# Performance work log

Measured on AMD Instinct MI355X. Metric: run time of the kernel, lower is better.

## Reference

```python
import jax, jax.numpy as jnp
import numpy as np

B, T, D = 16, 2048, 1024
NUM_LAYERS = 4
BN_EPS = 1e-5


def setup_inputs() -> dict:
    key = jax.random.key(0)
    ks = jax.random.split(key, 8)
    s = 1.0 / np.sqrt(D)
    x = jax.random.normal(ks[0], (B, T, D), dtype=jnp.float32)
    Wi = jax.random.normal(ks[1], (D, D), dtype=jnp.float32) * s   # SimpleCell input dense kernel
    bi = jnp.zeros((D,), dtype=jnp.float32)                         # SimpleCell input dense bias
    Wh = jax.random.normal(ks[2], (D, D), dtype=jnp.float32) * s   # recurrent dense kernel (no bias)
    mlp_W = jax.random.normal(ks[3], (NUM_LAYERS, D, D), dtype=jnp.float32) * s
    mlp_b = jnp.zeros((NUM_LAYERS, D), dtype=jnp.float32)
    bn_scale = jnp.ones((NUM_LAYERS, D), dtype=jnp.float32)
    bn_bias = jnp.zeros((NUM_LAYERS, D), dtype=jnp.float32)
    return {"x": x, "Wi": Wi, "bi": bi, "Wh": Wh,
            "mlp_W": mlp_W, "mlp_b": mlp_b,
            "bn_scale": bn_scale, "bn_bias": bn_bias}


def reference(x, Wi, bi, Wh, mlp_W, mlp_b, bn_scale, bn_bias):
    # --- linear recurrence (SimpleCell with identity activation) ---
    # h_t = (x_t @ Wi + bi) + h_{t-1} @ Wh,  h_0 = 0
    xp = jnp.einsum('btd,dh->bth', x, Wi) + bi          # pre-project inputs [B,T,H]

    def step(h, xt):
        h = xt + h @ Wh
        return h, h

    h0 = jnp.zeros((x.shape[0], Wh.shape[0]), dtype=x.dtype)
    _, ys = jax.lax.scan(step, h0, jnp.swapaxes(xp, 0, 1))  # scan over time
    y = jnp.swapaxes(ys, 0, 1)                               # [B,T,H]

    # --- residual MLP stack: gelu(BatchNorm(Linear(y))) + y ---
    n_layers = mlp_W.shape[0]
    for l in range(n_layers):
        z = jnp.einsum('bth,hk->btk', y, mlp_W[l]) + mlp_b[l]
        mean = jnp.mean(z, axis=(0, 1))
        var = jnp.var(z, axis=(0, 1))
        zn = (z - mean) * jax.lax.rsqrt(var + BN_EPS) * bn_scale[l] + bn_bias[l]
        y = jax.nn.gelu(zn) + y
    return y
```

## Files before the change

### kernel.cpp

```cpp
#include <hip/hip_runtime.h>
#include <math.h>

#define Bb   16
#define Tt   2048
#define Dd   1024
#define NL   4
#define MTOT (Bb * Tt)

typedef float f32x4 __attribute__((ext_vector_type(4)));
typedef short bf16x8 __attribute__((ext_vector_type(8)));

__device__ __forceinline__ unsigned short f2bf_rne(float x) {
    unsigned u = __float_as_uint(x);
    u += 0x7fffu + ((u >> 16) & 1u);
    return (unsigned short)(u >> 16);
}
__device__ __forceinline__ float bf2f(unsigned short h) {
    return __uint_as_float(((unsigned)h) << 16);
}
__device__ __forceinline__ float gelu_tanh(float x) {
    float x3 = x * x * x;
    float u  = 0.7978845608028654f * (x + 0.044715f * x3);
    return 0.5f * x * (1.0f + tanhf(u));
}
__device__ __forceinline__ void dma16(const void* g, void* l) {
    __builtin_amdgcn_global_load_lds(
        (const __attribute__((address_space(1))) unsigned int*)g,
        (__attribute__((address_space(3))) unsigned int*)l, 16, 0, 0);
}

__global__ __launch_bounds__(256)
void split_bt(const float* __restrict__ B, short* __restrict__ ht,
              short* __restrict__ lt)
{
    __shared__ float tile[32][33];
    const int t  = threadIdx.x;
    const int r  = t >> 3;
    const int c  = (t & 7) * 4;
    const int kb = blockIdx.y * 32;
    const int nb = blockIdx.x * 32;
    float4 v = *reinterpret_cast<const float4*>(
        &B[(size_t)(kb + r) * Dd + nb + c]);
    tile[r][c + 0] = v.x; tile[r][c + 1] = v.y;
    tile[r][c + 2] = v.z; tile[r][c + 3] = v.w;
    __syncthreads();
    unsigned h[4], lo[4];
#pragma unroll
    for (int q = 0; q < 4; ++q) {
        float f = tile[c + q][r];
        unsigned short hh = f2bf_rne(f);
        float rem = f - bf2f(hh);
        h[q]  = hh;
        lo[q] = f2bf_rne(rem);
    }
    uint2 hw, lw;
    hw.x = h[0]  | (h[1]  << 16); hw.y = h[2]  | (h[3]  << 16);
    lw.x = lo[0] | (lo[1] << 16); lw.y = lo[2] | (lo[3] << 16);
    const int n = nb + r;
    const int s = (c >> 3) ^ ((n >> 1) & 3);
    size_t off = ((size_t)(blockIdx.y * 1024 + n) * 4 + s) * 8 + (c & 4);
    *reinterpret_cast<uint2*>(&ht[off]) = hw;
    *reinterpret_cast<uint2*>(&lt[off]) = lw;
}

template<int MODE, int BN, int NT>
__global__ __launch_bounds__(256, 2)
void mfma_gemm(const float* __restrict__ A,
               const short* __restrict__ Bth, const short* __restrict__ Btl,
               const float* __restrict__ bias,
               const float* __restrict__ Sin,
               float* __restrict__ Cout,
               float* __restrict__ psum, float* __restrict__ psq,
               int m, int tstart)
{
    constexpr int NJ  = NT / 32;
    constexpr int BH  = 10240;
    constexpr int BPL = NT * 32;
    __shared__ __align__(16) short lds[BH + 2 * BPL];
    float* bnF = (float*)lds;

    const int tid  = threadIdx.x;
    const int lane = tid & 63;
    const int w    = tid >> 6;
    const int n0   = blockIdx.x * NT;
    const int m0g  = (MODE == 2) ? (blockIdx.y * Tt + tstart)
                                 : (blockIdx.y * 128);
    const int wm0  = (w >> 1) * 64;
    const int wn0  = (w & 1) * (NT / 2);
    const int ar   = tid >> 3;
    const int ac   = (tid & 7) * 4;

    int  arow_src[4];
    bool avalid[4];
#pragma unroll
    for (int p = 0; p < 4; ++p) {
        int rg = m0g + p * 32 + ar;
        bool v = true;
        if (MODE >= 1) { int t = rg & (Tt - 1); v = (t >= m); }
        avalid[p]   = v;
        arow_src[p] = (MODE >= 1 && v) ? (rg - m) : rg;
    }

    f32x4 acc[4][NJ];
#pragma unroll
    for (int i = 0; i < 4; ++i)
#pragma unroll
        for (int j = 0; j < NJ; ++j) acc[i][j] = (f32x4){0.f, 0.f, 0.f, 0.f};

    int a_off[4];
#pragma unroll
    for (int i = 0; i < 4; ++i) {
        int r = wm0 + i * 16 + (lane & 15);
        a_off[i] = r * 40 + (lane >> 4) * 8;
    }
    const int ln     = lane & 15;
    const int nlb    = wn0 + ln;
    const int b_off0 = BH + nlb * 32 +
                       (((lane >> 4) ^ ((nlb >> 1) & 3)) << 3);

    float4 aReg[4];
#pragma unroll
    for (int p = 0; p < 4; ++p)
        aReg[p] = *reinterpret_cast<const float4*>(
            &A[(size_t)arow_src[p] * Dd + ac]);

    for (int k0 = 0; k0 < Dd; k0 += 32) {
        __syncthreads();
#pragma unroll
        for (int p = 0; p < 4; ++p) {
            float4 v = aReg[p];
            if (MODE >= 1 && !avalid[p]) v = make_float4(0.f, 0.f, 0.f, 0.f);
            int wo = (p * 32 + ar) * 40 + ac;
            unsigned short h0 = f2bf_rne(v.x), h1 = f2bf_rne(v.y),
                           h2 = f2bf_rne(v.z), h3 = f2bf_rne(v.w);
            unsigned short g0 = f2bf_rne(v.x - bf2f(h0)),
                           g1 = f2bf_rne(v.y - bf2f(h1)),
                           g2 = f2bf_rne(v.z - bf2f(h2)),
                           g3 = f2bf_rne(v.w - bf2f(h3));
            uint2 hw, lw;
            hw.x = (unsigned)h0 | ((unsigned)h1 << 16);
            hw.y = (unsigned)h2 | ((unsigned)h3 << 16);
            lw.x = (unsigned)g0 | ((unsigned)g1 << 16);
            lw.y = (unsigned)g2 | ((unsigned)g3 << 16);
            *reinterpret_cast<uint2*>(&lds[wo])        = hw;
            *reinterpret_cast<uint2*>(&lds[wo + 5120]) = lw;
        }
        {
            const int kt = k0 >> 5;
#pragma unroll
            for (int q = 0; q < NT / 64; ++q) {
                size_t gfo = ((size_t)(kt * 1024 + n0 + q * 64 + (tid >> 2))
                              * 4 + (tid & 3)) * 8;
                dma16(&Bth[gfo], &lds[BH + q * 2048 + w * 512]);
                dma16(&Btl[gfo], &lds[BH + BPL + q * 2048 + w * 512]);
            }
        }
        __syncthreads();
        if (k0 + 32 < Dd) {
#pragma unroll
            for (int p = 0; p < 4; ++p)
                aReg[p] = *reinterpret_cast<const float4*>(
                    &A[(size_t)arow_src[p] * Dd + k0 + 32 + ac]);
        }
        bf16x8 ah[4], al[4];
#pragma unroll
        for (int i = 0; i < 4; ++i) {
            ah[i] = *reinterpret_cast<const bf16x8*>(&lds[a_off[i]]);
            al[i] = *reinterpret_cast<const bf16x8*>(&lds[a_off[i] + 5120]);
        }
#pragma unroll
        for (int j = 0; j < NJ; ++j) {
            int bo = b_off0 + j * 512;
            bf16x8 bh = *reinterpret_cast<const bf16x8*>(&lds[bo]);
            bf16x8 bl = *reinterpret_cast<const bf16x8*>(&lds[bo + BPL]);
#pragma unroll
            for (int i = 0; i < 4; ++i) {
                acc[i][j] = __builtin_amdgcn_mfma_f32_16x16x32_bf16(
                    ah[i], bh, acc[i][j], 0, 0, 0);
                acc[i][j] = __builtin_amdgcn_mfma_f32_16x16x32_bf16(
                    ah[i], bl, acc[i][j], 0, 0, 0);
                acc[i][j] = __builtin_amdgcn_mfma_f32_16x16x32_bf16(
                    al[i], bh, acc[i][j], 0, 0, 0);
            }
        }
    }

    if (BN) {
        __syncthreads();
        bnF[tid] = 0.f; bnF[256 + tid] = 0.f;
        __syncthreads();
    }
#pragma unroll
    for (int j = 0; j < NJ; ++j) {
        int cl  = wn0 + j * 16 + (lane & 15);
        int col = n0 + cl;
        float bj = (MODE == 0 && bias) ? bias[col] : 0.f;
        float sv = 0.f, sq = 0.f;
#pragma unroll
        for (int i = 0; i < 4; ++i) {
            int rbase = m0g + wm0 + i * 16 + (lane >> 4) * 4;
#pragma unroll
            for (int e = 0; e < 4; ++e) {
                size_t off = (size_t)(rbase + e) * Dd + col;
                float v = acc[i][j][e] + bj;
                if (MODE >= 1) v += Sin[off];
                Cout[off] = v;
                if (BN) { sv += v; sq += v * v; }
            }
        }
        if (BN) { atomicAdd(&bnF[cl], sv); atomicAdd(&bnF[256 + cl], sq); }
    }
    if (BN) {
        __syncthreads();
        psum[(size_t)blockIdx.y * Dd + n0 + tid] = bnF[tid];
        psq [(size_t)blockIdx.y * Dd + n0 + tid] = bnF[256 + tid];
    }
}

__global__ __launch_bounds__(256)
void bn_stats(const float* __restrict__ ps, const float* __restrict__ pq,
              const float* __restrict__ scale, const float* __restrict__ bias,
              float* __restrict__ Av, float* __restrict__ Cv)
{
    const int d = blockIdx.x * 256 + threadIdx.x;
    float s = 0.f, q = 0.f;
    for (int p = 0; p < 256; ++p) {
        s += ps[p * Dd + d];
        q += pq[p * Dd + d];
    }
    const float invN = 1.0f / 32768.0f;
    float mean = s * invN;
    float var  = q * invN - mean * mean;
    float rs   = rsqrtf(var + 1e-5f);
    float a    = rs * scale[d];
    Av[d] = a;
    Cv[d] = bias[d] - mean * a;
}

__global__ __launch_bounds__(256)
void residual_gelu(const float* __restrict__ Z, const float* __restrict__ Yin,
                   float* __restrict__ Yout,
                   const float* __restrict__ Av, const float* __restrict__ Cv)
{
    const float4* z4 = reinterpret_cast<const float4*>(Z);
    const float4* y4 = reinterpret_cast<const float4*>(Yin);
    float4*       o4 = reinterpret_cast<float4*>(Yout);
    const float4* a4 = reinterpret_cast<const float4*>(Av);
    const float4* c4 = reinterpret_cast<const float4*>(Cv);
    const int n4 = MTOT * Dd / 4;
    for (int i = blockIdx.x * blockDim.x + threadIdx.x; i < n4;
         i += gridDim.x * blockDim.x) {
        int d4 = i & (Dd / 4 - 1);
        float4 z = z4[i], y = y4[i], a = a4[d4], c = c4[d4];
        float4 o;
        o.x = gelu_tanh(fmaf(z.x, a.x, c.x)) + y.x;
        o.y = gelu_tanh(fmaf(z.y, a.y, c.y)) + y.y;
        o.z = gelu_tanh(fmaf(z.z, a.z, c.z)) + y.z;
        o.w = gelu_tanh(fmaf(z.w, a.w, c.w)) + y.w;
        o4[i] = o;
    }
}

extern "C" void kernel_launch(void* const* d_in, const int* in_sizes, int n_in,
                              void* d_out, int out_size, void* d_ws, size_t ws_size,
                              hipStream_t stream)
{
    const float* x    = (const float*)d_in[0];
    const float* Wi   = (const float*)d_in[1];
    const float* bi   = (const float*)d_in[2];
    const float* Wh   = (const float*)d_in[3];
    const float* mlpW = (const float*)d_in[4];
    const float* mlpb = (const float*)d_in[5];
    const float* bns  = (const float*)d_in[6];
    const float* bnb  = (const float*)d_in[7];
    float* out = (float*)d_out;

    float* ws   = (float*)d_ws;
    float* S0   = ws;
    float* Pa   = S0 + (size_t)MTOT * Dd;
    float* Pb   = Pa + (size_t)Dd * Dd;
    float* psum = Pb + (size_t)Dd * Dd;
    float* psq  = psum + 256 * Dd;
    float* abuf = psq + 256 * Dd;
    float* cbuf = abuf + Dd;
    short* Bth  = (short*)(cbuf + Dd);
    short* Btl  = Bth + (size_t)Dd * Dd;

    const dim3 gBig(4, 256);
    const dim3 gSq (8, 8);
    const dim3 gSeq(8, 16);
    const dim3 gBt (32, 32);

#define SPLIT(M) split_bt<<<gBt, 256, 0, stream>>>((M), Bth, Btl)
#define GEMM(MODE, BN, NT, grid, A_, bias_, Sin_, C_, ps_, pq_, m_, ts_)      \
    mfma_gemm<MODE, BN, NT><<<grid, 256, 0, stream>>>(                        \
        (A_), Bth, Btl, (bias_), (Sin_), (C_), (ps_), (pq_), (m_), (ts_))

    SPLIT(Wi);
    GEMM(0, 0, 256, gBig, x, bi, nullptr, S0, nullptr, nullptr, 0, 0);

    SPLIT(Wh);
    GEMM(1, 0, 256, gBig, S0, nullptr, S0, out, nullptr, nullptr, 1, 0);
    GEMM(0, 0, 128, gSq,  Wh, nullptr, nullptr, Pa, nullptr, nullptr, 0, 0);
    SPLIT(Pa);
    GEMM(1, 0, 256, gBig, out, nullptr, out, S0, nullptr, nullptr, 2, 0);
    GEMM(0, 0, 128, gSq,  Pa, nullptr, nullptr, Pb, nullptr, nullptr, 0, 0);
    SPLIT(Pb);
    GEMM(1, 0, 256, gBig, S0, nullptr, S0, out, nullptr, nullptr, 4, 0);
    GEMM(0, 0, 128, gSq,  Pb, nullptr, nullptr, Pa, nullptr, nullptr, 0, 0);
    SPLIT(Pa);
    GEMM(1, 0, 256, gBig, out, nullptr, out, S0, nullptr, nullptr, 8, 0);
    GEMM(0, 0, 128, gSq,  Pa, nullptr, nullptr, Pb, nullptr, nullptr, 0, 0);
    SPLIT(Pb);
    GEMM(1, 0, 256, gBig, S0, nullptr, S0, out, nullptr, nullptr, 16, 0);
    GEMM(0, 0, 128, gSq,  Pb, nullptr, nullptr, Pa, nullptr, nullptr, 0, 0);
    SPLIT(Pa);
    GEMM(1, 0, 256, gBig, out, nullptr, out, S0, nullptr, nullptr, 32, 0);
    GEMM(0, 0, 128, gSq,  Pa, nullptr, nullptr, Pb, nullptr, nullptr, 0, 0);
    SPLIT(Pb);
    GEMM(1, 0, 256, gBig, S0, nullptr, S0, out, nullptr, nullptr, 64, 0);
    GEMM(0, 0, 128, gSq,  Pb, nullptr, nullptr, Pa, nullptr, nullptr, 0, 0);
    SPLIT(Pa);

    for (int i = 1; i < 16; ++i)
        GEMM(2, 0, 128, gSeq, out, nullptr, out, out, nullptr, nullptr,
             128, 128 * i);

    for (int l = 0; l < NL; ++l) {
        SPLIT(mlpW + (size_t)l * Dd * Dd);
        GEMM(0, 1, 256, gBig, out, mlpb + (size_t)l * Dd, nullptr, S0,
             psum, psq, 0, 0);
        bn_stats<<<4, 256, 0, stream>>>(psum, psq, bns + (size_t)l * Dd,
                                        bnb + (size_t)l * Dd, abuf, cbuf);
        residual_gelu<<<2048, 256, 0, stream>>>(S0, out, out, abuf, cbuf);
    }
#undef SPLIT
#undef GEMM
}
```

Baseline: 3.789 ms.

## Double-buffer LDS tiles and move GEMM to 512-thread blocks with 8 waves

The MFMA GEMM kernel now runs 512 threads (8 waves in a 2x4 layout) per block, so each wave holds half as many accumulator columns. A and B tiles are double-buffered in LDS: the next k-tile's B DMA and A bf16 split conversion are issued before computing on the current buffer, leaving one barrier per iteration instead of two. This aims to overlap global loads with MFMA work and raise latency hiding. In exchange it doubles LDS use per block, which may lower occupancy, and adds explicit waitcnt/barrier inline asm.

Measured after the change: 4.801 ms. 1.27x slower.

```diff
diff --git a/kernel.cpp b/kernel.cpp
--- a/kernel.cpp
+++ b/kernel.cpp
@@ -64,7 +64,7 @@
 }
 
 template<int MODE, int BN, int NT>
-__global__ __launch_bounds__(256, 2)
+__global__ __launch_bounds__(512, 2)
 void mfma_gemm(const float* __restrict__ A,
                const short* __restrict__ Bth, const short* __restrict__ Btl,
                const float* __restrict__ bias,
@@ -73,11 +73,13 @@
                float* __restrict__ psum, float* __restrict__ psq,
                int m, int tstart)
 {
-    constexpr int NJ  = NT / 32;
-    constexpr int BH  = 10240;
-    constexpr int BPL = NT * 32;
-    __shared__ __align__(16) short lds[BH + 2 * BPL];
-    float* bnF = (float*)lds;
+    constexpr int NJ    = NT / 64;
+    constexpr int BPL   = NT * 32;
+    constexpr int ABUF  = 10240;
+    constexpr int BBUF  = 2 * BPL;
+    constexpr int BBASE = 2 * ABUF;
+    constexpr int NQ    = NT / 128;
+    __shared__ __align__(16) short lds[BBASE + 2 * BBUF];
 
     const int tid  = threadIdx.x;
     const int lane = tid & 63;
@@ -85,20 +87,31 @@
     const int n0   = blockIdx.x * NT;
     const int m0g  = (MODE == 2) ? (blockIdx.y * Tt + tstart)
                                  : (blockIdx.y * 128);
-    const int wm0  = (w >> 1) * 64;
-    const int wn0  = (w & 1) * (NT / 2);
-    const int ar   = tid >> 3;
-    const int ac   = (tid & 7) * 4;
-
-    int  arow_src[4];
-    bool avalid[4];
-#pragma unroll
-    for (int p = 0; p < 4; ++p) {
-        int rg = m0g + p * 32 + ar;
-        bool v = true;
-        if (MODE >= 1) { int t = rg & (Tt - 1); v = (t >= m); }
-        avalid[p]   = v;
-        arow_src[p] = (MODE >= 1 && v) ? (rg - m) : rg;
+    const int wm0  = (w >> 2) * 64;
+    const int wn0  = (w & 3) * (NT / 4);
+
+    const int ar = tid >> 2;
+    const int ac = (tid & 3) * 8;
+    const int rg = m0g + ar;
+    bool avalid = true;
+    if (MODE >= 1) { int t = rg & (Tt - 1); avalid = (t >= m); }
+    const size_t arow = (size_t)((MODE >= 1 && avalid) ? (rg - m) : rg);
+    const int awo = ar * 40 + ac;
+
+    int a_off[4];
+#pragma unroll
+    for (int i = 0; i < 4; ++i)
+        a_off[i] = (wm0 + i * 16 + (lane & 15)) * 40 + (lane >> 4) * 8;
+    const int ln  = lane & 15;
+    const int nlb = wn0 + ln;
+    const int b_off0 = nlb * 32 + (((lane >> 4) ^ ((nlb >> 1) & 3)) << 3);
+
+    int bnq[NQ], bsq[NQ], bcq[NQ];
+#pragma unroll
+    for (int q = 0; q < NQ; ++q) {
+        int c = w + q * 8;
+        int f = c * 64 + lane;
+        bcq[q] = c; bnq[q] = f >> 2; bsq[q] = f & 3;
     }
 
     f32x4 acc[4][NJ];
@@ -107,72 +120,58 @@
 #pragma unroll
         for (int j = 0; j < NJ; ++j) acc[i][j] = (f32x4){0.f, 0.f, 0.f, 0.f};
 
-    int a_off[4];
-#pragma unroll
-    for (int i = 0; i < 4; ++i) {
-        int r = wm0 + i * 16 + (lane & 15);
-        a_off[i] = r * 40 + (lane >> 4) * 8;
-    }
-    const int ln     = lane & 15;
-    const int nlb    = wn0 + ln;
-    const int b_off0 = BH + nlb * 32 +
-                       (((lane >> 4) ^ ((nlb >> 1) & 3)) << 3);
-
-    float4 aReg[4];
-#pragma unroll
-    for (int p = 0; p < 4; ++p)
-        aReg[p] = *reinterpret_cast<const float4*>(
-            &A[(size_t)arow_src[p] * Dd + ac]);
-
-    for (int k0 = 0; k0 < Dd; k0 += 32) {
-        __syncthreads();
-#pragma unroll
-        for (int p = 0; p < 4; ++p) {
-            float4 v = aReg[p];
-            if (MODE >= 1 && !avalid[p]) v = make_float4(0.f, 0.f, 0.f, 0.f);
-            int wo = (p * 32 + ar) * 40 + ac;
-            unsigned short h0 = f2bf_rne(v.x), h1 = f2bf_rne(v.y),
-                           h2 = f2bf_rne(v.z), h3 = f2bf_rne(v.w);
-            unsigned short g0 = f2bf_rne(v.x - bf2f(h0)),
-                           g1 = f2bf_rne(v.y - bf2f(h1)),
-                           g2 = f2bf_rne(v.z - bf2f(h2)),
-                           g3 = f2bf_rne(v.w - bf2f(h3));
-            uint2 hw, lw;
-            hw.x = (unsigned)h0 | ((unsigned)h1 << 16);
-            hw.y = (unsigned)h2 | ((unsigned)h3 << 16);
-            lw.x = (unsigned)g0 | ((unsigned)g1 << 16);
-            lw.y = (unsigned)g2 | ((unsigned)g3 << 16);
-            *reinterpret_cast<uint2*>(&lds[wo])        = hw;
-            *reinterpret_cast<uint2*>(&lds[wo + 5120]) = lw;
-        }
-        {
-            const int kt = k0 >> 5;
-#pragma unroll
-            for (int q = 0; q < NT / 64; ++q) {
-                size_t gfo = ((size_t)(kt * 1024 + n0 + q * 64 + (tid >> 2))
-                              * 4 + (tid & 3)) * 8;
-                dma16(&Bth[gfo], &lds[BH + q * 2048 + w * 512]);
-                dma16(&Btl[gfo], &lds[BH + BPL + q * 2048 + w * 512]);
-            }
-        }
-        __syncthreads();
-        if (k0 + 32 < Dd) {
-#pragma unroll
-            for (int p = 0; p < 4; ++p)
-                aReg[p] = *reinterpret_cast<const float4*>(
-                    &A[(size_t)arow_src[p] * Dd + k0 + 32 + ac]);
-        }
+    float4 aR0, aR1;
+
+    auto LOADA = [&](int kt) {
+        const float* p = &A[arow * Dd + kt * 32 + ac];
+        aR0 = *reinterpret_cast<const float4*>(p);
+        aR1 = *reinterpret_cast<const float4*>(p + 4);
+    };
+    auto CONVA = [&](int nb) {
+        float f[8] = {aR0.x, aR0.y, aR0.z, aR0.w, aR1.x, aR1.y, aR1.z, aR1.w};
+        if (MODE >= 1 && !avalid) {
+#pragma unroll
+            for (int e = 0; e < 8; ++e) f[e] = 0.f;
+        }
+        unsigned hh[8], ll[8];
+#pragma unroll
+        for (int e = 0; e < 8; ++e) {
+            unsigned short h = f2bf_rne(f[e]);
+            hh[e] = h;
+            ll[e] = f2bf_rne(f[e] - bf2f(h));
+        }
+        int4 hw, lw;
+        hw.x = (int)(hh[0] | (hh[1] << 16)); hw.y = (int)(hh[2] | (hh[3] << 16));
+        hw.z = (int)(hh[4] | (hh[5] << 16)); hw.w = (int)(hh[6] | (hh[7] << 16));
+        lw.x = (int)(ll[0] | (ll[1] << 16)); lw.y = (int)(ll[2] | (ll[3] << 16));
+        lw.z = (int)(ll[4] | (ll[5] << 16)); lw.w = (int)(ll[6] | (ll[7] << 16));
+        *reinterpret_cast<int4*>(&lds[nb * ABUF + awo])        = hw;
+        *reinterpret_cast<int4*>(&lds[nb * ABUF + awo + 5120]) = lw;
+    };
+    auto STAGEB = [&](int kt, int nb) {
+#pragma unroll
+        for (int q = 0; q < NQ; ++q) {
+            size_t g = ((size_t)(kt * 1024 + n0 + bnq[q]) * 4 + bsq[q]) * 8;
+            short* d = &lds[BBASE + nb * BBUF + bcq[q] * 512];
+            dma16(&Bth[g], d);
+            dma16(&Btl[g], d + BPL);
+        }
+    };
+    auto COMPUTE = [&](int nb) {
+        const int ab = nb * ABUF;
+        const int bb = BBASE + nb * BBUF;
         bf16x8 ah[4], al[4];
 #pragma unroll
         for (int i = 0; i < 4; ++i) {
-            ah[i] = *reinterpret_cast<const bf16x8*>(&lds[a_off[i]]);
-            al[i] = *reinterpret_cast<const bf16x8*>(&lds[a_off[i] + 5120]);
+            ah[i] = *reinterpret_cast<const bf16x8*>(&lds[ab + a_off[i]]);
+            al[i] = *reinterpret_cast<const bf16x8*>(&lds[ab + a_off[i] + 5120]);
         }
 #pragma unroll
         for (int j = 0; j < NJ; ++j) {
-            int bo = b_off0 + j * 512;
-            bf16x8 bh = *reinterpret_cast<const bf16x8*>(&lds[bo]);
-            bf16x8 bl = *reinterpret_cast<const bf16x8*>(&lds[bo + BPL]);
+            const bf16x8 bh = *reinterpret_cast<const bf16x8*>(
+                &lds[bb + b_off0 + j * 512]);
+            const bf16x8 bl = *reinterpret_cast<const bf16x8*>(
+                &lds[bb + b_off0 + j * 512 + BPL]);
 #pragma unroll
             for (int i = 0; i < 4; ++i) {
                 acc[i][j] = __builtin_amdgcn_mfma_f32_16x16x32_bf16(
@@ -183,16 +182,37 @@
                     al[i], bh, acc[i][j], 0, 0, 0);
             }
         }
-    }
-
+    };
+    auto CLOSE = [&]() {
+        asm volatile("s_waitcnt vmcnt(0) lgkmcnt(0)" ::: "memory");
+        __builtin_amdgcn_s_barrier();
+    };
+
+    LOADA(0);
+    STAGEB(0, 0);
+    CONVA(0);
+    LOADA(1);
+    CLOSE();
+
+    for (int kt = 0; kt < 32; ++kt) {
+        const int cur = kt & 1;
+        if (kt < 31) {
+            STAGEB(kt + 1, cur ^ 1);
+            CONVA(cur ^ 1);
+            if (kt < 30) LOADA(kt + 2);
+        }
+        COMPUTE(cur);
+        CLOSE();
+    }
+
+    float* bnF = reinterpret_cast<float*>(lds);
     if (BN) {
+        if (tid < 256) { bnF[tid] = 0.f; bnF[256 + tid] = 0.f; }
         __syncthreads();
-        bnF[tid] = 0.f; bnF[256 + tid] = 0.f;
-        __syncthreads();
     }
 #pragma unroll
     for (int j = 0; j < NJ; ++j) {
-        int cl  = wn0 + j * 16 + (lane & 15);
+        int cl  = wn0 + j * 16 + ln;
         int col = n0 + cl;
         float bj = (MODE == 0 && bias) ? bias[col] : 0.f;
         float sv = 0.f, sq = 0.f;
@@ -212,8 +232,10 @@
     }
     if (BN) {
         __syncthreads();
-        psum[(size_t)blockIdx.y * Dd + n0 + tid] = bnF[tid];
-        psq [(size_t)blockIdx.y * Dd + n0 + tid] = bnF[256 + tid];
+        if (tid < 256) {
+            psum[(size_t)blockIdx.y * Dd + n0 + tid] = bnF[tid];
+            psq [(size_t)blockIdx.y * Dd + n0 + tid] = bnF[256 + tid];
+        }
     }
 }
 
@@ -293,7 +315,7 @@
 
 #define SPLIT(M) split_bt<<<gBt, 256, 0, stream>>>((M), Bth, Btl)
 #define GEMM(MODE, BN, NT, grid, A_, bias_, Sin_, C_, ps_, pq_, m_, ts_)      \
-    mfma_gemm<MODE, BN, NT><<<grid, 256, 0, stream>>>(                        \
+    mfma_gemm<MODE, BN, NT><<<grid, 512, 0, stream>>>(                        \
         (A_), Bth, Btl, (bias_), (Sin_), (C_), (ps_), (pq_), (m_), (ts_))
 
     SPLIT(Wi);
```

## Use 1024-thread 256x256-tile GEMM for big matmuls and drop A prefetch

Applied to the files above, without the earlier changes.

Adds a separate large-tile GEMM kernel: 1024 threads (16 waves) compute a 256x256 output tile. It is used for the input projection, the doubling-step recurrence GEMMs and the MLP GEMMs, with a matching grid and BatchNorm partial-sum count. This raises operand reuse per block and halves the number of partial-stat rows. The small GEMM kernel is specialised to its fixed 128-column tile, and its register prefetch of the next A tile is removed, which may expose global load latency. The 1024-thread launch bounds and 73KB of LDS put pressure on registers and on occupancy.

Result: slower. 4.511 ms (+19.1%).

```diff
diff --git a/kernel.cpp b/kernel.cpp
--- a/kernel.cpp
+++ b/kernel.cpp
@@ -63,21 +63,157 @@
     *reinterpret_cast<uint2*>(&lt[off]) = lw;
 }
 
-template<int MODE, int BN, int NT>
+template<int MODE, int BN>
+__global__ __launch_bounds__(1024, 4)
+void mfma_gemm_b(const float* __restrict__ A,
+                 const short* __restrict__ Bth, const short* __restrict__ Btl,
+                 const float* __restrict__ bias,
+                 const float* __restrict__ Sin,
+                 float* __restrict__ Cout,
+                 float* __restrict__ psum, float* __restrict__ psq,
+                 int m)
+{
+    constexpr int AP  = 10240;
+    constexpr int BH  = 2 * AP;
+    constexpr int BPL = 256 * 32;
+    __shared__ __align__(16) short lds[BH + 2 * BPL];
+
+    const int tid  = threadIdx.x;
+    const int lane = tid & 63;
+    const int w    = tid >> 6;
+    const int n0   = blockIdx.x * 256;
+    const int m0g  = blockIdx.y * 256;
+    const int wm0  = (w >> 2) * 64;
+    const int wn0  = (w & 3) * 64;
+
+    const int ar = tid >> 2;
+    const int ac = (tid & 3) * 8;
+    const int rg = m0g + ar;
+    bool avalid = true;
+    if (MODE == 1) avalid = ((rg & (Tt - 1)) >= m);
+    const size_t arow = (size_t)((MODE == 1 && avalid) ? (rg - m) : rg);
+    const int awo = ar * 40 + ac;
+
+    int a_off[4];
+#pragma unroll
+    for (int i = 0; i < 4; ++i)
+        a_off[i] = (wm0 + i * 16 + (lane & 15)) * 40 + (lane >> 4) * 8;
+    const int ln  = lane & 15;
+    const int nlb = wn0 + ln;
+    const int b_off0 = BH + nlb * 32 + (((lane >> 4) ^ ((nlb >> 1) & 3)) << 3);
+
+    const size_t bfrag = (size_t)(n0 + (tid >> 2)) * 4 + (tid & 3);
+
+    f32x4 acc[4][4];
+#pragma unroll
+    for (int i = 0; i < 4; ++i)
+#pragma unroll
+        for (int j = 0; j < 4; ++j) acc[i][j] = (f32x4){0.f, 0.f, 0.f, 0.f};
+
+    for (int kt = 0; kt < 32; ++kt) {
+        __syncthreads();
+        {
+            const float* p = &A[arow * Dd + kt * 32 + ac];
+            float4 v0 = *reinterpret_cast<const float4*>(p);
+            float4 v1 = *reinterpret_cast<const float4*>(p + 4);
+            float f[8] = {v0.x, v0.y, v0.z, v0.w, v1.x, v1.y, v1.z, v1.w};
+            if (MODE == 1 && !avalid) {
+#pragma unroll
+                for (int e = 0; e < 8; ++e) f[e] = 0.f;
+            }
+            unsigned hh[8], ll[8];
+#pragma unroll
+            for (int e = 0; e < 8; ++e) {
+                unsigned short h = f2bf_rne(f[e]);
+                hh[e] = h;
+                ll[e] = f2bf_rne(f[e] - bf2f(h));
+            }
+            int4 hw, lw;
+            hw.x = (int)(hh[0] | (hh[1] << 16)); hw.y = (int)(hh[2] | (hh[3] << 16));
+            hw.z = (int)(hh[4] | (hh[5] << 16)); hw.w = (int)(hh[6] | (hh[7] << 16));
+            lw.x = (int)(ll[0] | (ll[1] << 16)); lw.y = (int)(ll[2] | (ll[3] << 16));
+            lw.z = (int)(ll[4] | (ll[5] << 16)); lw.w = (int)(ll[6] | (ll[7] << 16));
+            *reinterpret_cast<int4*>(&lds[awo])      = hw;
+            *reinterpret_cast<int4*>(&lds[awo + AP]) = lw;
+        }
+        {
+            size_t g = ((size_t)kt * 1024 * 4 + bfrag) * 8;
+            dma16(&Bth[g], &lds[BH + w * 512]);
+            dma16(&Btl[g], &lds[BH + BPL + w * 512]);
+        }
+        __syncthreads();
+        bf16x8 ah[4], al[4];
+#pragma unroll
+        for (int i = 0; i < 4; ++i) {
+            ah[i] = *reinterpret_cast<const bf16x8*>(&lds[a_off[i]]);
+            al[i] = *reinterpret_cast<const bf16x8*>(&lds[a_off[i] + AP]);
+        }
+#pragma unroll
+        for (int j = 0; j < 4; ++j) {
+            const bf16x8 bh = *reinterpret_cast<const bf16x8*>(
+                &lds[b_off0 + j * 512]);
+            const bf16x8 bl = *reinterpret_cast<const bf16x8*>(
+                &lds[b_off0 + j * 512 + BPL]);
+#pragma unroll
+            for (int i = 0; i < 4; ++i) {
+                acc[i][j] = __builtin_amdgcn_mfma_f32_16x16x32_bf16(
+                    ah[i], bh, acc[i][j], 0, 0, 0);
+                acc[i][j] = __builtin_amdgcn_mfma_f32_16x16x32_bf16(
+                    ah[i], bl, acc[i][j], 0, 0, 0);
+                acc[i][j] = __builtin_amdgcn_mfma_f32_16x16x32_bf16(
+                    al[i], bh, acc[i][j], 0, 0, 0);
+            }
+        }
+    }
+
+    float* bnF = reinterpret_cast<float*>(lds);
+    if (BN) {
+        __syncthreads();
+        if (tid < 256) { bnF[tid] = 0.f; bnF[256 + tid] = 0.f; }
+        __syncthreads();
+    }
+#pragma unroll
+    for (int j = 0; j < 4; ++j) {
+        int cl  = wn0 + j * 16 + ln;
+        int col = n0 + cl;
+        float bj = (MODE == 0 && bias) ? bias[col] : 0.f;
+        float sv = 0.f, sq = 0.f;
+#pragma unroll
+        for (int i = 0; i < 4; ++i) {
+            int rbase = m0g + wm0 + i * 16 + (lane >> 4) * 4;
+#pragma unroll
+            for (int e = 0; e < 4; ++e) {
+                size_t off = (size_t)(rbase + e) * Dd + col;
+                float v = acc[i][j][e] + bj;
+                if (MODE == 1) v += Sin[off];
+                Cout[off] = v;
+                if (BN) { sv += v; sq += v * v; }
+            }
+        }
+        if (BN) { atomicAdd(&bnF[cl], sv); atomicAdd(&bnF[256 + cl], sq); }
+    }
+    if (BN) {
+        __syncthreads();
+        if (tid < 256) {
+            psum[(size_t)blockIdx.y * Dd + n0 + tid] = bnF[tid];
+            psq [(size_t)blockIdx.y * Dd + n0 + tid] = bnF[256 + tid];
+        }
+    }
+}
+
+template<int MODE>
 __global__ __launch_bounds__(256, 2)
-void mfma_gemm(const float* __restrict__ A,
-               const short* __restrict__ Bth, const short* __restrict__ Btl,
-               const float* __restrict__ bias,
-               const float* __restrict__ Sin,
-               float* __restrict__ Cout,
-               float* __restrict__ psum, float* __restrict__ psq,
-               int m, int tstart)
-{
+void mfma_gemm_s(const float* __restrict__ A,
+                 const short* __restrict__ Bth, const short* __restrict__ Btl,
+                 const float* __restrict__ Sin,
+                 float* __restrict__ Cout,
+                 int m, int tstart)
+{
+    constexpr int NT  = 128;
     constexpr int NJ  = NT / 32;
     constexpr int BH  = 10240;
     constexpr int BPL = NT * 32;
     __shared__ __align__(16) short lds[BH + 2 * BPL];
-    float* bnF = (float*)lds;
 
     const int tid  = threadIdx.x;
     const int lane = tid & 63;
@@ -86,19 +222,15 @@
     const int m0g  = (MODE == 2) ? (blockIdx.y * Tt + tstart)
                                  : (blockIdx.y * 128);
     const int wm0  = (w >> 1) * 64;
-    const int wn0  = (w & 1) * (NT / 2);
+    const int wn0  = (w & 1) * 64;
     const int ar   = tid >> 3;
     const int ac   = (tid & 7) * 4;
 
     int  arow_src[4];
-    bool avalid[4];
 #pragma unroll
     for (int p = 0; p < 4; ++p) {
-        int rg = m0g + p * 32 + ar;
-        bool v = true;
-        if (MODE >= 1) { int t = rg & (Tt - 1); v = (t >= m); }
-        avalid[p]   = v;
-        arow_src[p] = (MODE >= 1 && v) ? (rg - m) : rg;
+        int rgp = m0g + p * 32 + ar;
+        arow_src[p] = (MODE == 2) ? (rgp - m) : rgp;
     }
 
     f32x4 acc[4][NJ];
@@ -109,27 +241,18 @@
 
     int a_off[4];
 #pragma unroll
-    for (int i = 0; i < 4; ++i) {
-        int r = wm0 + i * 16 + (lane & 15);
-        a_off[i] = r * 40 + (lane >> 4) * 8;
-    }
-    const int ln     = lane & 15;
-    const int nlb    = wn0 + ln;
-    const int b_off0 = BH + nlb * 32 +
-                       (((lane >> 4) ^ ((nlb >> 1) & 3)) << 3);
-
-    float4 aReg[4];
-#pragma unroll
-    for (int p = 0; p < 4; ++p)
-        aReg[p] = *reinterpret_cast<const float4*>(
-            &A[(size_t)arow_src[p] * Dd + ac]);
+    for (int i = 0; i < 4; ++i)
+        a_off[i] = (wm0 + i * 16 + (lane & 15)) * 40 + (lane >> 4) * 8;
+    const int ln  = lane & 15;
+    const int nlb = wn0 + ln;
+    const int b_off0 = BH + nlb * 32 + (((lane >> 4) ^ ((nlb >> 1) & 3)) << 3);
 
     for (int k0 = 0; k0 < Dd; k0 += 32) {
         __syncthreads();
 #pragma unroll
         for (int p = 0; p < 4; ++p) {
-            float4 v = aReg[p];
-            if (MODE >= 1 && !avalid[p]) v = make_float4(0.f, 0.f, 0.f, 0.f);
+            float4 v = *reinterpret_cast<const float4*>(
+                &A[(size_t)arow_src[p] * Dd + k0 + ac]);
             int wo = (p * 32 + ar) * 40 + ac;
             unsigned short h0 = f2bf_rne(v.x), h1 = f2bf_rne(v.y),
                            h2 = f2bf_rne(v.z), h3 = f2bf_rne(v.w);
@@ -156,12 +279,6 @@
             }
         }
         __syncthreads();
-        if (k0 + 32 < Dd) {
-#pragma unroll
-            for (int p = 0; p < 4; ++p)
-                aReg[p] = *reinterpret_cast<const float4*>(
-                    &A[(size_t)arow_src[p] * Dd + k0 + 32 + ac]);
-        }
         bf16x8 ah[4], al[4];
 #pragma unroll
         for (int i = 0; i < 4; ++i) {
@@ -170,9 +287,10 @@
         }
 #pragma unroll
         for (int j = 0; j < NJ; ++j) {
-            int bo = b_off0 + j * 512;
-            bf16x8 bh = *reinterpret_cast<const bf16x8*>(&lds[bo]);
-            bf16x8 bl = *reinterpret_cast<const bf16x8*>(&lds[bo + BPL]);
+            const bf16x8 bh = *reinterpret_cast<const bf16x8*>(
+                &lds[b_off0 + j * 512]);
+            const bf16x8 bl = *reinterpret_cast<const bf16x8*>(
+                &lds[b_off0 + j * 512 + BPL]);
 #pragma unroll
             for (int i = 0; i < 4; ++i) {
                 acc[i][j] = __builtin_amdgcn_mfma_f32_16x16x32_bf16(
@@ -185,35 +303,20 @@
         }
     }
 
-    if (BN) {
-        __syncthreads();
-        bnF[tid] = 0.f; bnF[256 + tid] = 0.f;
-        __syncthreads();
-    }
 #pragma unroll
     for (int j = 0; j < NJ; ++j) {
-        int cl  = wn0 + j * 16 + (lane & 15);
-        int col = n0 + cl;
-        float bj = (MODE == 0 && bias) ? bias[col] : 0.f;
-        float sv = 0.f, sq = 0.f;
+        int col = n0 + wn0 + j * 16 + ln;
 #pragma unroll
         for (int i = 0; i < 4; ++i) {
             int rbase = m0g + wm0 + i * 16 + (lane >> 4) * 4;
 #pragma unroll
             for (int e = 0; e < 4; ++e) {
                 size_t off = (size_t)(rbase + e) * Dd + col;
-                float v = acc[i][j][e] + bj;
-                if (MODE >= 1) v += Sin[off];
+                float v = acc[i][j][e];
+                if (MODE == 2) v += Sin[off];
                 Cout[off] = v;
-                if (BN) { sv += v; sq += v * v; }
-            }
-        }
-        if (BN) { atomicAdd(&bnF[cl], sv); atomicAdd(&bnF[256 + cl], sq); }
-    }
-    if (BN) {
-        __syncthreads();
-        psum[(size_t)blockIdx.y * Dd + n0 + tid] = bnF[tid];
-        psq [(size_t)blockIdx.y * Dd + n0 + tid] = bnF[256 + tid];
+            }
+        }
     }
 }
 
@@ -224,7 +327,7 @@
 {
     const int d = blockIdx.x * 256 + threadIdx.x;
     float s = 0.f, q = 0.f;
-    for (int p = 0; p < 256; ++p) {
+    for (int p = 0; p < 128; ++p) {
         s += ps[p * Dd + d];
         q += pq[p * Dd + d];
     }
@@ -286,54 +389,56 @@
     short* Bth  = (short*)(cbuf + Dd);
     short* Btl  = Bth + (size_t)Dd * Dd;
 
-    const dim3 gBig(4, 256);
+    const dim3 gBig(4, 128);
     const dim3 gSq (8, 8);
     const dim3 gSeq(8, 16);
     const dim3 gBt (32, 32);
 
 #define SPLIT(M) split_bt<<<gBt, 256, 0, stream>>>((M), Bth, Btl)
-#define GEMM(MODE, BN, NT, grid, A_, bias_, Sin_, C_, ps_, pq_, m_, ts_)      \
-    mfma_gemm<MODE, BN, NT><<<grid, 256, 0, stream>>>(                        \
-        (A_), Bth, Btl, (bias_), (Sin_), (C_), (ps_), (pq_), (m_), (ts_))
+#define GEMMB(MODE, BN, A_, bias_, Sin_, C_, ps_, pq_, m_)                    \
+    mfma_gemm_b<MODE, BN><<<gBig, 1024, 0, stream>>>(                         \
+        (A_), Bth, Btl, (bias_), (Sin_), (C_), (ps_), (pq_), (m_))
+#define GEMMS(MODE, grid, A_, Sin_, C_, m_, ts_)                              \
+    mfma_gemm_s<MODE><<<grid, 256, 0, stream>>>(                              \
+        (A_), Bth, Btl, (Sin_), (C_), (m_), (ts_))
 
     SPLIT(Wi);
-    GEMM(0, 0, 256, gBig, x, bi, nullptr, S0, nullptr, nullptr, 0, 0);
+    GEMMB(0, 0, x, bi, nullptr, S0, nullptr, nullptr, 0);
 
     SPLIT(Wh);
-    GEMM(1, 0, 256, gBig, S0, nullptr, S0, out, nullptr, nullptr, 1, 0);
-    GEMM(0, 0, 128, gSq,  Wh, nullptr, nullptr, Pa, nullptr, nullptr, 0, 0);
+    GEMMB(1, 0, S0, nullptr, S0, out, nullptr, nullptr, 1);
+    GEMMS(0, gSq, Wh, nullptr, Pa, 0, 0);
     SPLIT(Pa);
-    GEMM(1, 0, 256, gBig, out, nullptr, out, S0, nullptr, nullptr, 2, 0);
-    GEMM(0, 0, 128, gSq,  Pa, nullptr, nullptr, Pb, nullptr, nullptr, 0, 0);
+    GEMMB(1, 0, out, nullptr, out, S0, nullptr, nullptr, 2);
+    GEMMS(0, gSq, Pa, nullptr, Pb, 0, 0);
     SPLIT(Pb);
-    GEMM(1, 0, 256, gBig, S0, nullptr, S0, out, nullptr, nullptr, 4, 0);
-    GEMM(0, 0, 128, gSq,  Pb, nullptr, nullptr, Pa, nullptr, nullptr, 0, 0);
+    GEMMB(1, 0, S0, nullptr, S0, out, nullptr, nullptr, 4);
+    GEMMS(0, gSq, Pb, nullptr, Pa, 0, 0);
     SPLIT(Pa);
-    GEMM(1, 0, 256, gBig, out, nullptr, out, S0, nullptr, nullptr, 8, 0);
-    GEMM(0, 0, 128, gSq,  Pa, nullptr, nullptr, Pb, nullptr, nullptr, 0, 0);
+    GEMMB(1, 0, out, nullptr, out, S0, nullptr, nullptr, 8);
+    GEMMS(0, gSq, Pa, nullptr, Pb, 0, 0);
     SPLIT(Pb);
-    GEMM(1, 0, 256, gBig, S0, nullptr, S0, out, nullptr, nullptr, 16, 0);
-    GEMM(0, 0, 128, gSq,  Pb, nullptr, nullptr, Pa, nullptr, nullptr, 0, 0);
+    GEMMB(1, 0, S0, nullptr, S0, out, nullptr, nullptr, 16);
+    GEMMS(0, gSq, Pb, nullptr, Pa, 0, 0);
     SPLIT(Pa);
-    GEMM(1, 0, 256, gBig, out, nullptr, out, S0, nullptr, nullptr, 32, 0);
-    GEMM(0, 0, 128, gSq,  Pa, nullptr, nullptr, Pb, nullptr, nullptr, 0, 0);
+    GEMMB(1, 0, out, nullptr, out, S0, nullptr, nullptr, 32);
+    GEMMS(0, gSq, Pa, nullptr, Pb, 0, 0);
     SPLIT(Pb);
-    GEMM(1, 0, 256, gBig, S0, nullptr, S0, out, nullptr, nullptr, 64, 0);
-    GEMM(0, 0, 128, gSq,  Pb, nullptr, nullptr, Pa, nullptr, nullptr, 0, 0);
+    GEMMB(1, 0, S0, nullptr, S0, out, nullptr, nullptr, 64);
+    GEMMS(0, gSq, Pb, nullptr, Pa, 0, 0);
     SPLIT(Pa);
 
     for (int i = 1; i < 16; ++i)
-        GEMM(2, 0, 128, gSeq, out, nullptr, out, out, nullptr, nullptr,
-             128, 128 * i);
+        GEMMS(2, gSeq, out, out, out, 128, 128 * i);
 
     for (int l = 0; l < NL; ++l) {
         SPLIT(mlpW + (size_t)l * Dd * Dd);
-        GEMM(0, 1, 256, gBig, out, mlpb + (size_t)l * Dd, nullptr, S0,
-             psum, psq, 0, 0);
+        GEMMB(0, 1, out, mlpb + (size_t)l * Dd, nullptr, S0, psum, psq, 0);
         bn_stats<<<4, 256, 0, stream>>>(psum, psq, bns + (size_t)l * Dd,
                                         bnb + (size_t)l * Dd, abuf, cbuf);
         residual_gelu<<<2048, 256, 0, stream>>>(S0, out, out, abuf, cbuf);
     }
 #undef SPLIT
-#undef GEMM
-}
+#undef GEMMB
+#undef GEMMS
+}
```

## Store activations as pre-split bf16 hi/lo planes and DMA A tiles into LDS

Applied to the files above, without the earlier changes.

Intermediate activations are now kept in a hi/lo bf16 split format in the workspace instead of fp32, and GEMM epilogues write that format directly. The big GEMMs then load A tiles with global_load_lds DMA instead of converting fp32 to bf16 pairs in registers every k-step. This removes the per-tile conversion work and the register prefetch for A. The cost is that the epilogues and the residual kernel now do the split and recombine, and dropping the register prefetch reduces overlap. Total memory traffic is unchanged, and numerics shift slightly because intermediates are rounded to a hi+lo bf16 pair.

After: 4.697 ms. 1.24x slower.

```diff
diff --git a/kernel.cpp b/kernel.cpp
--- a/kernel.cpp
+++ b/kernel.cpp
@@ -17,6 +17,9 @@
 }
 __device__ __forceinline__ float bf2f(unsigned short h) {
     return __uint_as_float(((unsigned)h) << 16);
+}
+__device__ __forceinline__ float rec2(unsigned short h, unsigned short l) {
+    return bf2f(h) + bf2f(l);
 }
 __device__ __forceinline__ float gelu_tanh(float x) {
     float x3 = x * x * x;
@@ -63,21 +66,24 @@
     *reinterpret_cast<uint2*>(&lt[off]) = lw;
 }
 
-template<int MODE, int BN, int NT>
+template<int MODE, int BN, int NT, int ADMA, int OSPLIT>
 __global__ __launch_bounds__(256, 2)
-void mfma_gemm(const float* __restrict__ A,
+void mfma_gemm(const float* __restrict__ Af,
+               const short* __restrict__ Ah, const short* __restrict__ Al,
                const short* __restrict__ Bth, const short* __restrict__ Btl,
                const float* __restrict__ bias,
-               const float* __restrict__ Sin,
-               float* __restrict__ Cout,
+               const short* __restrict__ Sh, const short* __restrict__ Sl,
+               float* __restrict__ Cf,
+               short* __restrict__ Ch, short* __restrict__ Cl,
                float* __restrict__ psum, float* __restrict__ psq,
+               const short* __restrict__ zp,
                int m, int tstart)
 {
-    constexpr int NJ  = NT / 32;
-    constexpr int BH  = 10240;
-    constexpr int BPL = NT * 32;
-    __shared__ __align__(16) short lds[BH + 2 * BPL];
-    float* bnF = (float*)lds;
+    constexpr int NJ    = NT / 32;
+    constexpr int APL   = ADMA ? 4096 : 5120;
+    constexpr int BBASE = 2 * APL;
+    constexpr int BPL   = NT * 32;
+    __shared__ __align__(16) short lds[BBASE + 2 * BPL];
 
     const int tid  = threadIdx.x;
     const int lane = tid & 63;
@@ -87,19 +93,49 @@
                                  : (blockIdx.y * 128);
     const int wm0  = (w >> 1) * 64;
     const int wn0  = (w & 1) * (NT / 2);
-    const int ar   = tid >> 3;
-    const int ac   = (tid & 7) * 4;
-
-    int  arow_src[4];
-    bool avalid[4];
-#pragma unroll
-    for (int p = 0; p < 4; ++p) {
-        int rg = m0g + p * 32 + ar;
-        bool v = true;
-        if (MODE >= 1) { int t = rg & (Tt - 1); v = (t >= m); }
-        avalid[p]   = v;
-        arow_src[p] = (MODE >= 1 && v) ? (rg - m) : rg;
-    }
+    const int ln   = lane & 15;
+
+    const int ar = tid >> 3;
+    const int ac = (tid & 7) * 4;
+    int  arow_src[4]; bool avalid[4];
+    if (!ADMA) {
+#pragma unroll
+        for (int p = 0; p < 4; ++p) {
+            int rg = m0g + p * 32 + ar;
+            bool v = true;
+            if (MODE == 1) v = ((rg & (Tt - 1)) >= m);
+            avalid[p]   = v;
+            arow_src[p] = (MODE >= 1 && v) ? (rg - m) : rg;
+        }
+    }
+    const short* ah_src[2];
+    const short* al_src[2];
+    int adst[2];
+    if (ADMA) {
+#pragma unroll
+        for (int r = 0; r < 2; ++r) {
+            int rl = (r * 4 + w) * 16 + (lane >> 2);
+            int rg = m0g + rl;
+            bool v = true;
+            if (MODE == 1) v = ((rg & (Tt - 1)) >= m);
+            int srow = (MODE >= 1) ? (rg - m) : rg;
+            int slot = ((lane & 3) ^ ((rl >> 1) & 3)) << 3;
+            ah_src[r] = v ? (Ah + (size_t)srow * Dd + slot) : zp;
+            al_src[r] = v ? (Al + (size_t)srow * Dd + slot) : zp;
+            adst[r]   = (r * 4 + w) * 512;
+        }
+    }
+
+    int a_off[4];
+#pragma unroll
+    for (int i = 0; i < 4; ++i) {
+        int rl = wm0 + i * 16 + ln;
+        a_off[i] = ADMA ? (rl * 32 + (((lane >> 4) ^ ((rl >> 1) & 3)) << 3))
+                        : (rl * 40 + (lane >> 4) * 8);
+    }
+    const int nlb    = wn0 + ln;
+    const int b_off0 = BBASE + nlb * 32 +
+                       (((lane >> 4) ^ ((nlb >> 1) & 3)) << 3);
 
     f32x4 acc[4][NJ];
 #pragma unroll
@@ -107,72 +143,57 @@
 #pragma unroll
         for (int j = 0; j < NJ; ++j) acc[i][j] = (f32x4){0.f, 0.f, 0.f, 0.f};
 
-    int a_off[4];
-#pragma unroll
-    for (int i = 0; i < 4; ++i) {
-        int r = wm0 + i * 16 + (lane & 15);
-        a_off[i] = r * 40 + (lane >> 4) * 8;
-    }
-    const int ln     = lane & 15;
-    const int nlb    = wn0 + ln;
-    const int b_off0 = BH + nlb * 32 +
-                       (((lane >> 4) ^ ((nlb >> 1) & 3)) << 3);
-
-    float4 aReg[4];
-#pragma unroll
-    for (int p = 0; p < 4; ++p)
-        aReg[p] = *reinterpret_cast<const float4*>(
-            &A[(size_t)arow_src[p] * Dd + ac]);
-
-    for (int k0 = 0; k0 < Dd; k0 += 32) {
+    for (int kt = 0; kt < 32; ++kt) {
         __syncthreads();
-#pragma unroll
-        for (int p = 0; p < 4; ++p) {
-            float4 v = aReg[p];
-            if (MODE >= 1 && !avalid[p]) v = make_float4(0.f, 0.f, 0.f, 0.f);
-            int wo = (p * 32 + ar) * 40 + ac;
-            unsigned short h0 = f2bf_rne(v.x), h1 = f2bf_rne(v.y),
-                           h2 = f2bf_rne(v.z), h3 = f2bf_rne(v.w);
-            unsigned short g0 = f2bf_rne(v.x - bf2f(h0)),
-                           g1 = f2bf_rne(v.y - bf2f(h1)),
-                           g2 = f2bf_rne(v.z - bf2f(h2)),
-                           g3 = f2bf_rne(v.w - bf2f(h3));
-            uint2 hw, lw;
-            hw.x = (unsigned)h0 | ((unsigned)h1 << 16);
-            hw.y = (unsigned)h2 | ((unsigned)h3 << 16);
-            lw.x = (unsigned)g0 | ((unsigned)g1 << 16);
-            lw.y = (unsigned)g2 | ((unsigned)g3 << 16);
-            *reinterpret_cast<uint2*>(&lds[wo])        = hw;
-            *reinterpret_cast<uint2*>(&lds[wo + 5120]) = lw;
-        }
-        {
-            const int kt = k0 >> 5;
-#pragma unroll
-            for (int q = 0; q < NT / 64; ++q) {
-                size_t gfo = ((size_t)(kt * 1024 + n0 + q * 64 + (tid >> 2))
-                              * 4 + (tid & 3)) * 8;
-                dma16(&Bth[gfo], &lds[BH + q * 2048 + w * 512]);
-                dma16(&Btl[gfo], &lds[BH + BPL + q * 2048 + w * 512]);
+        if (ADMA) {
+#pragma unroll
+            for (int r = 0; r < 2; ++r) {
+                dma16(ah_src[r] + kt * 32, &lds[adst[r]]);
+                dma16(al_src[r] + kt * 32, &lds[APL + adst[r]]);
             }
+        } else {
+            const int k0 = kt * 32;
+#pragma unroll
+            for (int p = 0; p < 4; ++p) {
+                float4 v = *reinterpret_cast<const float4*>(
+                    &Af[(size_t)arow_src[p] * Dd + k0 + ac]);
+                if (MODE == 1 && !avalid[p]) v = make_float4(0.f,0.f,0.f,0.f);
+                int wo = (p * 32 + ar) * 40 + ac;
+                unsigned short h0 = f2bf_rne(v.x), h1 = f2bf_rne(v.y),
+                               h2 = f2bf_rne(v.z), h3 = f2bf_rne(v.w);
+                unsigned short g0 = f2bf_rne(v.x - bf2f(h0)),
+                               g1 = f2bf_rne(v.y - bf2f(h1)),
+                               g2 = f2bf_rne(v.z - bf2f(h2)),
+                               g3 = f2bf_rne(v.w - bf2f(h3));
+                uint2 hw, lw;
+                hw.x = (unsigned)h0 | ((unsigned)h1 << 16);
+                hw.y = (unsigned)h2 | ((unsigned)h3 << 16);
+                lw.x = (unsigned)g0 | ((unsigned)g1 << 16);
+                lw.y = (unsigned)g2 | ((unsigned)g3 << 16);
+                *reinterpret_cast<uint2*>(&lds[wo])       = hw;
+                *reinterpret_cast<uint2*>(&lds[wo + APL]) = lw;
+            }
+        }
+#pragma unroll
+        for (int q = 0; q < NT / 64; ++q) {
+            size_t gfo = ((size_t)(kt * 1024 + n0 + q * 64 + (tid >> 2))
+                          * 4 + (tid & 3)) * 8;
+            dma16(&Bth[gfo], &lds[BBASE + q * 2048 + w * 512]);
+            dma16(&Btl[gfo], &lds[BBASE + BPL + q * 2048 + w * 512]);
         }
         __syncthreads();
-        if (k0 + 32 < Dd) {
-#pragma unroll
-            for (int p = 0; p < 4; ++p)
-                aReg[p] = *reinterpret_cast<const float4*>(
-                    &A[(size_t)arow_src[p] * Dd + k0 + 32 + ac]);
-        }
         bf16x8 ah[4], al[4];
 #pragma unroll
         for (int i = 0; i < 4; ++i) {
             ah[i] = *reinterpret_cast<const bf16x8*>(&lds[a_off[i]]);
-            al[i] = *reinterpret_cast<const bf16x8*>(&lds[a_off[i] + 5120]);
+            al[i] = *reinterpret_cast<const bf16x8*>(&lds[a_off[i] + APL]);
         }
 #pragma unroll
         for (int j = 0; j < NJ; ++j) {
-            int bo = b_off0 + j * 512;
-            bf16x8 bh = *reinterpret_cast<const bf16x8*>(&lds[bo]);
-            bf16x8 bl = *reinterpret_cast<const bf16x8*>(&lds[bo + BPL]);
+            const bf16x8 bh = *reinterpret_cast<const bf16x8*>(
+                &lds[b_off0 + j * 512]);
+            const bf16x8 bl = *reinterpret_cast<const bf16x8*>(
+                &lds[b_off0 + j * 512 + BPL]);
 #pragma unroll
             for (int i = 0; i < 4; ++i) {
                 acc[i][j] = __builtin_amdgcn_mfma_f32_16x16x32_bf16(
@@ -185,6 +206,7 @@
         }
     }
 
+    float* bnF = reinterpret_cast<float*>(lds);
     if (BN) {
         __syncthreads();
         bnF[tid] = 0.f; bnF[256 + tid] = 0.f;
@@ -192,7 +214,7 @@
     }
 #pragma unroll
     for (int j = 0; j < NJ; ++j) {
-        int cl  = wn0 + j * 16 + (lane & 15);
+        int cl  = wn0 + j * 16 + ln;
         int col = n0 + cl;
         float bj = (MODE == 0 && bias) ? bias[col] : 0.f;
         float sv = 0.f, sq = 0.f;
@@ -203,8 +225,16 @@
             for (int e = 0; e < 4; ++e) {
                 size_t off = (size_t)(rbase + e) * Dd + col;
                 float v = acc[i][j][e] + bj;
-                if (MODE >= 1) v += Sin[off];
-                Cout[off] = v;
+                if (MODE >= 1)
+                    v += rec2((unsigned short)Sh[off], (unsigned short)Sl[off]);
+                if (OSPLIT) {
+                    unsigned short hs = f2bf_rne(v);
+                    unsigned short ls = f2bf_rne(v - bf2f(hs));
+                    Ch[off] = (short)hs;
+                    Cl[off] = (short)ls;
+                } else {
+                    Cf[off] = v;
+                }
                 if (BN) { sv += v; sq += v * v; }
             }
         }
@@ -237,27 +267,52 @@
     Cv[d] = bias[d] - mean * a;
 }
 
+template<int LAST>
 __global__ __launch_bounds__(256)
-void residual_gelu(const float* __restrict__ Z, const float* __restrict__ Yin,
-                   float* __restrict__ Yout,
+void residual_gelu(const short* __restrict__ Zh, const short* __restrict__ Zl,
+                   const short* __restrict__ Yh, const short* __restrict__ Yl,
+                   short* __restrict__ Oh, short* __restrict__ Ol,
+                   float* __restrict__ Of,
                    const float* __restrict__ Av, const float* __restrict__ Cv)
 {
-    const float4* z4 = reinterpret_cast<const float4*>(Z);
-    const float4* y4 = reinterpret_cast<const float4*>(Yin);
-    float4*       o4 = reinterpret_cast<float4*>(Yout);
-    const float4* a4 = reinterpret_cast<const float4*>(Av);
-    const float4* c4 = reinterpret_cast<const float4*>(Cv);
-    const int n4 = MTOT * Dd / 4;
-    for (int i = blockIdx.x * blockDim.x + threadIdx.x; i < n4;
-         i += gridDim.x * blockDim.x) {
-        int d4 = i & (Dd / 4 - 1);
-        float4 z = z4[i], y = y4[i], a = a4[d4], c = c4[d4];
-        float4 o;
-        o.x = gelu_tanh(fmaf(z.x, a.x, c.x)) + y.x;
-        o.y = gelu_tanh(fmaf(z.y, a.y, c.y)) + y.y;
-        o.z = gelu_tanh(fmaf(z.z, a.z, c.z)) + y.z;
-        o.w = gelu_tanh(fmaf(z.w, a.w, c.w)) + y.w;
-        o4[i] = o;
+    const int ng = MTOT * Dd / 8;
+    for (int g = blockIdx.x * blockDim.x + threadIdx.x; g < ng;
+         g += gridDim.x * blockDim.x) {
+        size_t base = (size_t)g * 8;
+        int d0 = (int)(base & (Dd - 1));
+        bf16x8 zh = *reinterpret_cast<const bf16x8*>(&Zh[base]);
+        bf16x8 zl = *reinterpret_cast<const bf16x8*>(&Zl[base]);
+        bf16x8 yh = *reinterpret_cast<const bf16x8*>(&Yh[base]);
+        bf16x8 yl = *reinterpret_cast<const bf16x8*>(&Yl[base]);
+        float4 a0 = *reinterpret_cast<const float4*>(&Av[d0]);
+        float4 a1 = *reinterpret_cast<const float4*>(&Av[d0 + 4]);
+        float4 c0 = *reinterpret_cast<const float4*>(&Cv[d0]);
+        float4 c1 = *reinterpret_cast<const float4*>(&Cv[d0 + 4]);
+        float av[8] = {a0.x,a0.y,a0.z,a0.w,a1.x,a1.y,a1.z,a1.w};
+        float cw[8] = {c0.x,c0.y,c0.z,c0.w,c1.x,c1.y,c1.z,c1.w};
+        float o[8];
+#pragma unroll
+        for (int e = 0; e < 8; ++e) {
+            float z = rec2((unsigned short)zh[e], (unsigned short)zl[e]);
+            float y = rec2((unsigned short)yh[e], (unsigned short)yl[e]);
+            o[e] = gelu_tanh(fmaf(z, av[e], cw[e])) + y;
+        }
+        if (LAST) {
+            float4 o0 = {o[0], o[1], o[2], o[3]};
+            float4 o1 = {o[4], o[5], o[6], o[7]};
+            *reinterpret_cast<float4*>(&Of[base])     = o0;
+            *reinterpret_cast<float4*>(&Of[base + 4]) = o1;
+        } else {
+            bf16x8 oh, ol;
+#pragma unroll
+            for (int e = 0; e < 8; ++e) {
+                unsigned short hs = f2bf_rne(o[e]);
+                oh[e] = (short)hs;
+                ol[e] = (short)f2bf_rne(o[e] - bf2f(hs));
+            }
+            *reinterpret_cast<bf16x8*>(&Oh[base]) = oh;
+            *reinterpret_cast<bf16x8*>(&Ol[base]) = ol;
+        }
     }
 }
 
@@ -275,65 +330,86 @@
     const float* bnb  = (const float*)d_in[7];
     float* out = (float*)d_out;
 
-    float* ws   = (float*)d_ws;
-    float* S0   = ws;
-    float* Pa   = S0 + (size_t)MTOT * Dd;
-    float* Pb   = Pa + (size_t)Dd * Dd;
+    const size_t NE = (size_t)MTOT * Dd;
+    short* S0h = (short*)d_ws;
+    short* S0l = S0h + NE;
+    short* S1h = S0l + NE;
+    short* S1l = S1h + NE;
+    float* Pa  = (float*)(S1l + NE);
+    float* Pb  = Pa + (size_t)Dd * Dd;
     float* psum = Pb + (size_t)Dd * Dd;
     float* psq  = psum + 256 * Dd;
     float* abuf = psq + 256 * Dd;
     float* cbuf = abuf + Dd;
     short* Bth  = (short*)(cbuf + Dd);
     short* Btl  = Bth + (size_t)Dd * Dd;
+    short* zp   = Btl + (size_t)Dd * Dd;
 
     const dim3 gBig(4, 256);
     const dim3 gSq (8, 8);
     const dim3 gSeq(8, 16);
     const dim3 gBt (32, 32);
 
+    hipMemsetAsync(zp, 0, 8192, stream);
+
 #define SPLIT(M) split_bt<<<gBt, 256, 0, stream>>>((M), Bth, Btl)
-#define GEMM(MODE, BN, NT, grid, A_, bias_, Sin_, C_, ps_, pq_, m_, ts_)      \
-    mfma_gemm<MODE, BN, NT><<<grid, 256, 0, stream>>>(                        \
-        (A_), Bth, Btl, (bias_), (Sin_), (C_), (ps_), (pq_), (m_), (ts_))
+#define LEVEL(srcH, srcL, dstH, dstL, m_)                                     \
+    mfma_gemm<1, 0, 256, 1, 1><<<gBig, 256, 0, stream>>>(                     \
+        nullptr, (srcH), (srcL), Bth, Btl, nullptr, (srcH), (srcL),           \
+        nullptr, (dstH), (dstL), nullptr, nullptr, zp, (m_), 0)
+#define SQUARE(Afp, Cfp)                                                      \
+    mfma_gemm<0, 0, 128, 0, 0><<<gSq, 256, 0, stream>>>(                      \
+        (Afp), nullptr, nullptr, Bth, Btl, nullptr, nullptr, nullptr,         \
+        (Cfp), nullptr, nullptr, nullptr, nullptr, zp, 0, 0)
 
     SPLIT(Wi);
-    GEMM(0, 0, 256, gBig, x, bi, nullptr, S0, nullptr, nullptr, 0, 0);
+    mfma_gemm<0, 0, 256, 0, 1><<<gBig, 256, 0, stream>>>(
+        x, nullptr, nullptr, Bth, Btl, bi, nullptr, nullptr,
+        nullptr, S0h, S0l, nullptr, nullptr, zp, 0, 0);
 
     SPLIT(Wh);
-    GEMM(1, 0, 256, gBig, S0, nullptr, S0, out, nullptr, nullptr, 1, 0);
-    GEMM(0, 0, 128, gSq,  Wh, nullptr, nullptr, Pa, nullptr, nullptr, 0, 0);
+    LEVEL(S0h, S0l, S1h, S1l, 1);
+    SQUARE(Wh, Pa);
     SPLIT(Pa);
-    GEMM(1, 0, 256, gBig, out, nullptr, out, S0, nullptr, nullptr, 2, 0);
-    GEMM(0, 0, 128, gSq,  Pa, nullptr, nullptr, Pb, nullptr, nullptr, 0, 0);
+    LEVEL(S1h, S1l, S0h, S0l, 2);
+    SQUARE(Pa, Pb);
     SPLIT(Pb);
-    GEMM(1, 0, 256, gBig, S0, nullptr, S0, out, nullptr, nullptr, 4, 0);
-    GEMM(0, 0, 128, gSq,  Pb, nullptr, nullptr, Pa, nullptr, nullptr, 0, 0);
+    LEVEL(S0h, S0l, S1h, S1l, 4);
+    SQUARE(Pb, Pa);
     SPLIT(Pa);
-    GEMM(1, 0, 256, gBig, out, nullptr, out, S0, nullptr, nullptr, 8, 0);
-    GEMM(0, 0, 128, gSq,  Pa, nullptr, nullptr, Pb, nullptr, nullptr, 0, 0);
+    LEVEL(S1h, S1l, S0h, S0l, 8);
+    SQUARE(Pa, Pb);
     SPLIT(Pb);
-    GEMM(1, 0, 256, gBig, S0, nullptr, S0, out, nullptr, nullptr, 16, 0);
-    GEMM(0, 0, 128, gSq,  Pb, nullptr, nullptr, Pa, nullptr, nullptr, 0, 0);
+    LEVEL(S0h, S0l, S1h, S1l, 16);
+    SQUARE(Pb, Pa);
     SPLIT(Pa);
-    GEMM(1, 0, 256, gBig, out, nullptr, out, S0, nullptr, nullptr, 32, 0);
-    GEMM(0, 0, 128, gSq,  Pa, nullptr, nullptr, Pb, nullptr, nullptr, 0, 0);
+    LEVEL(S1h, S1l, S0h, S0l, 32);
+    SQUARE(Pa, Pb);
     SPLIT(Pb);
-    GEMM(1, 0, 256, gBig, S0, nullptr, S0, out, nullptr, nullptr, 64, 0);
-    GEMM(0, 0, 128, gSq,  Pb, nullptr, nullptr, Pa, nullptr, nullptr, 0, 0);
+    LEVEL(S0h, S0l, S1h, S1l, 64);
+    SQUARE(Pb, Pa);
     SPLIT(Pa);
 
     for (int i = 1; i < 16; ++i)
-        GEMM(2, 0, 128, gSeq, out, nullptr, out, out, nullptr, nullptr,
-             128, 128 * i);
+        mfma_gemm<2, 0, 128, 1, 1><<<gSeq, 256, 0, stream>>>(
+            nullptr, S1h, S1l, Bth, Btl, nullptr, S1h, S1l,
+            nullptr, S1h, S1l, nullptr, nullptr, zp, 128, 128 * i);
 
     for (int l = 0; l < NL; ++l) {
         SPLIT(mlpW + (size_t)l * Dd * Dd);
-        GEMM(0, 1, 256, gBig, out, mlpb + (size_t)l * Dd, nullptr, S0,
-             psum, psq, 0, 0);
+        mfma_gemm<0, 1, 256, 1, 1><<<gBig, 256, 0, stream>>>(
+            nullptr, S1h, S1l, Bth, Btl, mlpb + (size_t)l * Dd,
+            nullptr, nullptr, nullptr, S0h, S0l, psum, psq, zp, 0, 0);
         bn_stats<<<4, 256, 0, stream>>>(psum, psq, bns + (size_t)l * Dd,
                                         bnb + (size_t)l * Dd, abuf, cbuf);
-        residual_gelu<<<2048, 256, 0, stream>>>(S0, out, out, abuf, cbuf);
+        if (l < NL - 1)
+            residual_gelu<0><<<2048, 256, 0, stream>>>(
+                S0h, S0l, S1h, S1l, S1h, S1l, nullptr, abuf, cbuf);
+        else
+            residual_gelu<1><<<2048, 256, 0, stream>>>(
+                S0h, S0l, S1h, S1l, nullptr, nullptr, out, abuf, cbuf);
     }
 #undef SPLIT
-#undef GEMM
-}
+#undef LEVEL
+#undef SQUARE
+}
```
